# Optimization experiments

Measured on AMD Instinct MI355X. Metric: run time of the kernel, lower is better.

The kernel has to match this reference:

```python
import jax, jax.numpy as jnp
import numpy as np

ATT_DIM = 512
HEADS = 8
HEAD_DIM = ATT_DIM // HEADS
D_IN = 512
LEFT_MASK = 256
RIGHT_MASK = 0
LARGE = 1e30


def pos_encoding(S, d):
    # Transformer-XL sinusoid table over relative positions S-1 .. -(S-1), length 2S-1.
    inv_freq = (1.0 / (10000.0 ** (np.arange(0, d, 2.0) / d))).astype(np.float32)
    pos = jnp.arange(S - 1, -S, -1, dtype=jnp.float32)          # [2S-1]
    ang = pos[:, None] * jnp.asarray(inv_freq)[None, :]          # [2S-1, d/2]
    # concat([sin, cos], -1) on a trailing singleton -> interleaved sin/cos per frequency
    return jnp.stack([jnp.sin(ang), jnp.cos(ang)], axis=-1).reshape(2 * S - 1, d)


def rel_shift(x):
    # x: [B, N, S, 2S-1] -> [B, N, S, S] with out[i, j] = x[i, S-1 - i + j]
    B, N, S, L = x.shape
    x = jnp.pad(x, ((0, 0), (0, 0), (0, 0), (1, 0)))             # [B,N,S,L+1]
    x = x.reshape(B, N, L + 1, S)[:, :, 1:, :]                   # [B,N,L,S]
    x = x.reshape(B, N, S, L)
    return x[:, :, :, :S]


def setup_inputs() -> dict:
    key = jax.random.key(0)
    ks = jax.random.split(key, 9)
    B, S, D = 2, 2048, D_IN
    scale = 0.02
    return {
        "x": jax.random.normal(ks[0], (B, S, D), dtype=jnp.float32),
        "Wq": jax.random.normal(ks[1], (D, ATT_DIM), dtype=jnp.float32) * scale,
        "b_con": jax.random.normal(ks[2], (ATT_DIM,), dtype=jnp.float32) * scale,
        "b_rel": jax.random.normal(ks[3], (ATT_DIM,), dtype=jnp.float32) * scale,
        "Wk": jax.random.normal(ks[4], (D, ATT_DIM), dtype=jnp.float32) * scale,
        "Wkr": jax.random.normal(ks[5], (D_IN, ATT_DIM), dtype=jnp.float32) * scale,
        "Wv": jax.random.normal(ks[6], (D, ATT_DIM), dtype=jnp.float32) * scale,
        "bv": jax.random.normal(ks[7], (ATT_DIM,), dtype=jnp.float32) * scale,
        "x_len": jax.random.randint(ks[8], (B,), 1, S + 1).astype(jnp.int32),
    }


def reference(x, Wq, b_con, b_rel, Wk, Wkr, Wv, bv, x_len):
    B, S, D = x.shape
    N, Dh = HEADS, HEAD_DIM

    # content/relative query share the kernel (TiedDense) with separate biases
    q_lin = jnp.einsum('bsd,de->bse', x, Wq)
    q_con = (q_lin + b_con).reshape(B, S, N, Dh)
    q_rel = (q_lin + b_rel).reshape(B, S, N, Dh)
    k_con = jnp.einsum('bsd,de->bse', x, Wk).reshape(B, S, N, Dh)

    content_energy = jnp.einsum('bind,bjnd->bnij', q_con, k_con)  # [B,N,S,S]

    pos_emb = pos_encoding(S, D_IN)                               # [2S-1, D]
    k_rel = (pos_emb @ Wkr).reshape(2 * S - 1, N, Dh)
    relative_energy = jnp.einsum('bind,jnd->bnij', q_rel, k_rel)  # [B,N,S,2S-1]
    relative_energy = rel_shift(relative_energy)                  # [B,N,S,S]

    energy = (content_energy + relative_energy) / jnp.sqrt(jnp.float32(Dh))

    # sequence mask over keys (broadcast [B,1,1,S]) * banded mask (band_part)
    j = jnp.arange(S)
    seq_mask = (j[None, :] < x_len[:, None]).astype(jnp.float32)[:, None, None, :]
    i = jnp.arange(S)[:, None]
    band = ((i - j[None, :] <= LEFT_MASK) & (j[None, :] - i <= RIGHT_MASK)).astype(jnp.float32)
    mask = seq_mask * band[None, None, :, :]

    masked_energy = energy - (1.0 - mask) * LARGE
    attention = jax.nn.softmax(masked_energy, axis=-1)

    v = (jnp.einsum('bsd,de->bse', x, Wv) + bv).reshape(B, S, N, Dh)
    context = jnp.einsum('bnij,bjnd->bind', attention, v).reshape(B, S, N * Dh)
    return context
```

## Files before the change

### kernel.cpp

```cpp
#include <hip/hip_runtime.h>
#include <math.h>

#define S_ 2048
#define NH 8
#define DH 64
#define CSL 320
#define LP 72

typedef __attribute__((ext_vector_type(8))) short short8;
typedef __attribute__((ext_vector_type(4))) float f32x4;
typedef unsigned short ushort_t;

__device__ __forceinline__ short bf16r(float x) {
    union { float f; unsigned u; } v; v.f = x;
    unsigned r = v.u + 0x7fffu + ((v.u >> 16) & 1u);
    return (short)(r >> 16);
}
__device__ __forceinline__ float b2f(ushort_t h) {
    union { float f; unsigned u; } v; v.u = ((unsigned)h) << 16; return v.f;
}

__global__ __launch_bounds__(256) void prep_kernel(
    const float* __restrict__ x,
    const float* __restrict__ Wq, const float* __restrict__ Wk,
    const float* __restrict__ Wv, const float* __restrict__ Wkr,
    ushort_t* __restrict__ WTq, ushort_t* __restrict__ WTk,
    ushort_t* __restrict__ WTv, ushort_t* __restrict__ WTkr,
    ushort_t* __restrict__ pos, ushort_t* __restrict__ xb16)
{
    const int widx = blockIdx.z;
    const int t = threadIdx.x;
    if (widx == 4) {
        const int base = blockIdx.y * 8 + blockIdx.x;
        const float C = -0.051905126482615036f;
        const int f = t;
#pragma unroll
        for (int rep = 0; rep < 6; ++rep) {
            const int r = base + rep * 64;
            unsigned pk = 0;
            if (r <= 256) {
                float ang = (float)r * exp2f(C * (float)f);
                unsigned s = (unsigned)(ushort_t)bf16r(sinf(ang));
                unsigned c = (unsigned)(ushort_t)bf16r(cosf(ang));
                pk = s | (c << 16);
            }
            ((unsigned*)pos)[(size_t)r * 256 + f] = pk;
        }
        return;
    }
    if (widx == 5) {
        const int sub = blockIdx.y * 8 + blockIdx.x;
        const size_t base = (size_t)sub * 32768;
#pragma unroll
        for (int it = 0; it < 8; ++it) {
            const size_t idx = base + (size_t)it * 4096 + (size_t)t * 16;
            const float* src = &x[idx];
            ushort_t t16[16];
#pragma unroll
            for (int u = 0; u < 16; ++u) t16[u] = (ushort_t)bf16r(src[u]);
            *(short8*)&xb16[idx]     = *(short8*)&t16[0];
            *(short8*)&xb16[idx + 8] = *(short8*)&t16[8];
        }
        return;
    }
    const float* W = (widx == 0) ? Wq : (widx == 1) ? Wk : (widx == 2) ? Wv : Wkr;
    ushort_t* WT   = (widx == 0) ? WTq : (widx == 1) ? WTk : (widx == 2) ? WTv : WTkr;
    const int k0 = blockIdx.x * 64, n0 = blockIdx.y * 64;
    __shared__ __align__(16) ushort_t T[64][72];
    const int srow = t >> 2, sc0 = (t & 3) * 16;
    const float* src = &W[(size_t)(k0 + srow) * 512 + n0 + sc0];
#pragma unroll
    for (int u = 0; u < 16; ++u) T[sc0 + u][srow] = (ushort_t)bf16r(src[u]);
    __syncthreads();
    ushort_t* dst = &WT[(size_t)(n0 + srow) * 512 + k0 + sc0];
    *(short8*)dst       = *(const short8*)&T[srow][sc0];
    *(short8*)(dst + 8) = *(const short8*)&T[srow][sc0 + 8];
}

__global__ __launch_bounds__(256) void qkv_gemm(
    const ushort_t* __restrict__ xb16,
    const ushort_t* __restrict__ WTq, const ushort_t* __restrict__ WTk,
    const ushort_t* __restrict__ WTv,
    const ushort_t* __restrict__ pos, const ushort_t* __restrict__ WTkr,
    const float* __restrict__ b_con, const float* __restrict__ b_rel,
    const float* __restrict__ bv,
    ushort_t* __restrict__ qcon, ushort_t* __restrict__ qrel,
    ushort_t* __restrict__ kout, ushort_t* __restrict__ vT,
    ushort_t* __restrict__ krel)
{
    const int widx = blockIdx.y >> 3;
    const int tid = threadIdx.x, lane = tid & 63, w = tid >> 6;
    const int quad = lane >> 4, l16 = lane & 15;

    __shared__ __align__(16) ushort_t A_lds[128][40];
    __shared__ __align__(16) ushort_t B_lds[64][40];

    f32x4 acc[2][4];
#pragma unroll
    for (int mt = 0; mt < 2; ++mt)
#pragma unroll
        for (int nt = 0; nt < 4; ++nt) acc[mt][nt] = (f32x4){0.f, 0.f, 0.f, 0.f};

    const int arow = tid >> 1, ak0 = (tid & 1) * 16;
    const int brow = tid >> 2, bk0 = (tid & 3) * 8;

    if (widx < 2) {
        const int m0 = blockIdx.x * 128;
        const int n0 = (blockIdx.y & 7) * 64;
        const ushort_t* WT = (widx == 0) ? WTq : WTk;
        const ushort_t* xrow = &xb16[(size_t)(m0 + arow) * 512 + ak0];
        const ushort_t* wrow = &WT[(size_t)(n0 + brow) * 512 + bk0];

        short8 pa0 = *(const short8*)xrow;
        short8 pa1 = *(const short8*)(xrow + 8);
        short8 pb  = *(const short8*)wrow;

#pragma unroll 1
        for (int k0 = 0; k0 < 512; k0 += 32) {
            __syncthreads();
            *(short8*)&A_lds[arow][ak0]     = pa0;
            *(short8*)&A_lds[arow][ak0 + 8] = pa1;
            *(short8*)&B_lds[brow][bk0]     = pb;
            if (k0 < 480) {
                pa0 = *(const short8*)(xrow + k0 + 32);
                pa1 = *(const short8*)(xrow + k0 + 40);
                pb  = *(const short8*)(wrow + k0 + 32);
            }
            __syncthreads();
            short8 a0 = *(const short8*)&A_lds[w * 32 + l16][quad * 8];
            short8 a1 = *(const short8*)&A_lds[w * 32 + 16 + l16][quad * 8];
#pragma unroll
            for (int nt = 0; nt < 4; ++nt) {
                short8 bb = *(const short8*)&B_lds[nt * 16 + l16][quad * 8];
                acc[0][nt] = __builtin_amdgcn_mfma_f32_16x16x32_bf16(a0, bb, acc[0][nt], 0, 0, 0);
                acc[1][nt] = __builtin_amdgcn_mfma_f32_16x16x32_bf16(a1, bb, acc[1][nt], 0, 0, 0);
            }
        }

#pragma unroll
        for (int nt = 0; nt < 4; ++nt) {
            const int col = n0 + nt * 16 + l16;
            float bc = 0.f, br = 0.f;
            if (widx == 0) { bc = b_con[col]; br = b_rel[col]; }
#pragma unroll
            for (int mt = 0; mt < 2; ++mt) {
#pragma unroll
                for (int reg = 0; reg < 4; ++reg) {
                    const size_t m = (size_t)(m0 + w * 32 + mt * 16 + quad * 4 + reg);
                    const float val = acc[mt][nt][reg];
                    if (widx == 0) {
                        qcon[m * 512 + col] = (ushort_t)bf16r((val + bc) * 0.125f);
                        qrel[m * 512 + col] = (ushort_t)bf16r((val + br) * 0.125f);
                    } else {
                        kout[m * 512 + col] = (ushort_t)bf16r(val);
                    }
                }
            }
        }
    } else if (widx == 2) {
        const int vb = (blockIdx.y & 7) * 32 + blockIdx.x;
        const int m0d = (vb & 3) * 128;
        const int n0j = (vb >> 2) * 64;
        const ushort_t* wrow = &WTv[(size_t)(m0d + arow) * 512 + ak0];
        const ushort_t* xrow = &xb16[(size_t)(n0j + brow) * 512 + bk0];

        short8 pa0 = *(const short8*)wrow;
        short8 pa1 = *(const short8*)(wrow + 8);
        short8 pb  = *(const short8*)xrow;

#pragma unroll 1
        for (int k0 = 0; k0 < 512; k0 += 32) {
            __syncthreads();
            *(short8*)&A_lds[arow][ak0]     = pa0;
            *(short8*)&A_lds[arow][ak0 + 8] = pa1;
            *(short8*)&B_lds[brow][bk0]     = pb;
            if (k0 < 480) {
                pa0 = *(const short8*)(wrow + k0 + 32);
                pa1 = *(const short8*)(wrow + k0 + 40);
                pb  = *(const short8*)(xrow + k0 + 32);
            }
            __syncthreads();
            short8 a0 = *(const short8*)&A_lds[w * 32 + l16][quad * 8];
            short8 a1 = *(const short8*)&A_lds[w * 32 + 16 + l16][quad * 8];
#pragma unroll
            for (int nt = 0; nt < 4; ++nt) {
                short8 bb = *(const short8*)&B_lds[nt * 16 + l16][quad * 8];
                acc[0][nt] = __builtin_amdgcn_mfma_f32_16x16x32_bf16(a0, bb, acc[0][nt], 0, 0, 0);
                acc[1][nt] = __builtin_amdgcn_mfma_f32_16x16x32_bf16(a1, bb, acc[1][nt], 0, 0, 0);
            }
        }

        const int b = n0j >> 11;
#pragma unroll
        for (int mt = 0; mt < 2; ++mt) {
#pragma unroll
            for (int reg = 0; reg < 4; ++reg) {
                const int d = m0d + w * 32 + mt * 16 + quad * 4 + reg;
                const int n = d >> 6, dd = d & 63;
                const float bvv = bv[d];
#pragma unroll
                for (int nt = 0; nt < 4; ++nt) {
                    const int s = (n0j + nt * 16 + l16) & 2047;
                    vT[((size_t)((b * NH + n) * 64 + dd)) * 2048 + s] =
                        (ushort_t)bf16r(acc[mt][nt][reg] + bvv);
                }
            }
        }
    } else {
        if (blockIdx.x >= 24) return;
        const int m0 = (blockIdx.x >> 3) * 128;
        const int n0 = (blockIdx.x & 7) * 64;
        const ushort_t* prow = &pos[(size_t)(m0 + arow) * 512 + ak0];
        const ushort_t* wrow = &WTkr[(size_t)(n0 + brow) * 512 + bk0];

        short8 pa0 = *(const short8*)prow;
        short8 pa1 = *(const short8*)(prow + 8);
        short8 pb  = *(const short8*)wrow;

#pragma unroll 1
        for (int k0 = 0; k0 < 512; k0 += 32) {
            __syncthreads();
            *(short8*)&A_lds[arow][ak0]     = pa0;
            *(short8*)&A_lds[arow][ak0 + 8] = pa1;
            *(short8*)&B_lds[brow][bk0]     = pb;
            if (k0 < 480) {
                pa0 = *(const short8*)(prow + k0 + 32);
                pa1 = *(const short8*)(prow + k0 + 40);
                pb  = *(const short8*)(wrow + k0 + 32);
            }
            __syncthreads();
            short8 a0 = *(const short8*)&A_lds[w * 32 + l16][quad * 8];
            short8 a1 = *(const short8*)&A_lds[w * 32 + 16 + l16][quad * 8];
#pragma unroll
            for (int nt = 0; nt < 4; ++nt) {
                short8 bb = *(const short8*)&B_lds[nt * 16 + l16][quad * 8];
                acc[0][nt] = __builtin_amdgcn_mfma_f32_16x16x32_bf16(a0, bb, acc[0][nt], 0, 0, 0);
                acc[1][nt] = __builtin_amdgcn_mfma_f32_16x16x32_bf16(a1, bb, acc[1][nt], 0, 0, 0);
            }
        }

#pragma unroll
        for (int nt = 0; nt < 4; ++nt) {
            const int col = n0 + nt * 16 + l16;
#pragma unroll
            for (int mt = 0; mt < 2; ++mt)
#pragma unroll
                for (int reg = 0; reg < 4; ++reg) {
                    const size_t m = (size_t)(m0 + w * 32 + mt * 16 + quad * 4 + reg);
                    krel[m * 512 + col] = (ushort_t)bf16r(acc[mt][nt][reg]);
                }
        }
    }
}

__global__ __launch_bounds__(256) void rel_gemm(
    const ushort_t* __restrict__ qrel, const ushort_t* __restrict__ krel,
    const ushort_t* __restrict__ vT, ushort_t* __restrict__ R3,
    float* __restrict__ vmean)
{
    const int tile = blockIdx.x, n = blockIdx.y, b = blockIdx.z;
    const int tid = threadIdx.x, lane = tid & 63, w = tid >> 6;
    const int quad = lane >> 4, l16 = lane & 15;

    __shared__ __align__(16) ushort_t A_lds[128][LP];
    __shared__ __align__(16) ushort_t B_lds[64][LP];

    if (tile == 16) {
        const int row = tid >> 2, seg = tid & 3;
        const ushort_t* src = &vT[((size_t)((b * NH + n) * 64 + row)) * 2048 + seg * 512];
        float sum = 0.f;
        for (int it = 0; it < 64; ++it) {
            short8 h = *(const short8*)(src + it * 8);
#pragma unroll
            for (int u = 0; u < 8; ++u) sum += b2f((ushort_t)h[u]);
        }
        float* scratch = (float*)A_lds;
        scratch[row * 4 + seg] = sum;
        __syncthreads();
        if (tid < 64) {
            float s = scratch[tid * 4] + scratch[tid * 4 + 1]
                    + scratch[tid * 4 + 2] + scratch[tid * 4 + 3];
            vmean[(size_t)b * 512 + n * 64 + tid] = s * (1.0f / (float)S_);
        }
        return;
    }

    const int i0 = tile * 128;
    {
        const int srow = tid >> 1, sc0 = (tid & 1) * 32;
        const ushort_t* src = &qrel[((size_t)b * S_ + i0 + srow) * 512 + n * 64 + sc0];
#pragma unroll
        for (int u = 0; u < 4; ++u)
            *(short8*)&A_lds[srow][sc0 + u * 8] = *(const short8*)(src + u * 8);
    }

    const size_t rbase3 = (size_t)(b * NH + n) * S_ * CSL;
    const int srow2 = tid >> 2, sc2 = (tid & 3) * 16;

    short8 pb0, pb1;
    auto issueB = [&](int rc) {
        const ushort_t* src = &krel[(size_t)(rc * 64 + srow2) * 512 + n * 64 + sc2];
        pb0 = *(const short8*)src;
        pb1 = *(const short8*)(src + 8);
    };
    issueB(0);

#pragma unroll 1
    for (int rc = 0; rc < 5; ++rc) {
        __syncthreads();
        *(short8*)&B_lds[srow2][sc2]     = pb0;
        *(short8*)&B_lds[srow2][sc2 + 8] = pb1;
        if (rc < 4) issueB(rc + 1);
        __syncthreads();

        short8 a[2][2];
#pragma unroll
        for (int mt = 0; mt < 2; ++mt) {
            a[mt][0] = *(const short8*)&A_lds[w * 32 + mt * 16 + l16][quad * 8];
            a[mt][1] = *(const short8*)&A_lds[w * 32 + mt * 16 + l16][quad * 8 + 32];
        }
#pragma unroll
        for (int nt = 0; nt < 4; ++nt) {
            short8 b0 = *(const short8*)&B_lds[nt * 16 + l16][quad * 8];
            short8 b1 = *(const short8*)&B_lds[nt * 16 + l16][quad * 8 + 32];
            const int r = rc * 64 + nt * 16 + l16;
#pragma unroll
            for (int mt = 0; mt < 2; ++mt) {
                f32x4 s = (f32x4){0.f, 0.f, 0.f, 0.f};
                s = __builtin_amdgcn_mfma_f32_16x16x32_bf16(a[mt][0], b0, s, 0, 0, 0);
                s = __builtin_amdgcn_mfma_f32_16x16x32_bf16(a[mt][1], b1, s, 0, 0, 0);
                if (r <= 256) {
#pragma unroll
                    for (int reg = 0; reg < 4; ++reg) {
                        const int ig = i0 + w * 32 + mt * 16 + quad * 4 + reg;
                        const int cslot = (ig & 31) + 256 - r;
                        R3[rbase3 + (size_t)ig * CSL + cslot] = (ushort_t)bf16r(s[reg]);
                    }
                }
            }
        }
    }
}

__global__ __launch_bounds__(128) void attn_kernel(
    const ushort_t* __restrict__ qcon, const ushort_t* __restrict__ kbuf,
    const ushort_t* __restrict__ vT, const ushort_t* __restrict__ R3,
    const float* __restrict__ vmean, const int* __restrict__ xlen_p,
    float* __restrict__ out)
{
    const int bx = blockIdx.x;
    const int tile = ((bx & 7) << 3) | (bx >> 3);
    const int n = blockIdx.y, b = blockIdx.z;
    const int i0 = tile * 32;
    const int tid = threadIdx.x, lane = tid & 63, w = tid >> 6;
    const int quad = lane >> 4, l16 = lane & 15;
    const int xlen = xlen_p[b];

    __shared__ __align__(16) ushort_t q_lds[32][LP];
    __shared__ __align__(16) ushort_t k_lds[64][LP];
    __shared__ __align__(16) ushort_t vT_lds[64][LP];
    __shared__ __align__(16) ushort_t p_lds[32][LP];
    __shared__ __align__(16) ushort_t Rl_lds[32][LP];

    {
        const int qr = tid >> 2, qc = (tid & 3) * 16;
        const ushort_t* src = &qcon[((size_t)b * S_ + i0 + qr) * 512 + n * 64 + qc];
        *(short8*)&q_lds[qr][qc]     = *(const short8*)src;
        *(short8*)&q_lds[qr][qc + 8] = *(const short8*)(src + 8);
    }

    f32x4 Oa[4];
#pragma unroll
    for (int nt = 0; nt < 4; ++nt) Oa[nt] = (f32x4){0.f, 0.f, 0.f, 0.f};
    float lpart[4] = {};

    const size_t rbase3 = (size_t)(b * NH + n) * S_ * CSL;
    const size_t vTbase = (size_t)((b * NH + n) * 64) * 2048;
    const int srow = tid >> 1, sc0 = (tid & 1) * 32;
    const int rrow = tid >> 2, rcol = (tid & 3) * 16;
    const short8 z8 = {0, 0, 0, 0, 0, 0, 0, 0};

    short8 kr[4], vr[4], kn[4], vn[4];
    short8 rcur[2], rnxt[2];

    auto issue = [&](int c, short8* kd, short8* vd, short8* rd) {
        const int jc0 = i0 - 256 + c * 64;
        const int jg = jc0 + srow;
        const bool okk = (jg >= 0);
        const ushort_t* ks = &kbuf[((size_t)b * S_ + jg) * 512 + n * 64 + sc0];
        const ushort_t* vs = &vT[vTbase + (size_t)srow * 2048 + jc0 + sc0];
#pragma unroll
        for (int u = 0; u < 4; ++u) {
            kd[u] = okk ? *(const short8*)(ks + u * 8) : z8;
            const bool okv = (jc0 + sc0 + u * 8) >= 0;
            vd[u] = okv ? *(const short8*)(vs + u * 8) : z8;
        }
        const ushort_t* Rs = &R3[rbase3 + (size_t)(i0 + rrow) * CSL + c * 64 + rcol];
        rd[0] = *(const short8*)Rs;
        rd[1] = *(const short8*)(Rs + 8);
    };

    issue(0, kr, vr, rcur);

#pragma unroll 1
    for (int c = 0; c < 5; ++c) {
        const int jc0 = i0 - 256 + c * 64;
        __syncthreads();
#pragma unroll
        for (int u = 0; u < 4; ++u) {
            *(short8*)&k_lds[srow][sc0 + u * 8]  = kr[u];
            *(short8*)&vT_lds[srow][sc0 + u * 8] = vr[u];
        }
        *(short8*)&Rl_lds[rrow][rcol]     = rcur[0];
        *(short8*)&Rl_lds[rrow][rcol + 8] = rcur[1];
        if (c < 4) issue(c + 1, kn, vn, rnxt);
        __syncthreads();

        short8 aq0 = *(const short8*)&q_lds[w * 16 + l16][quad * 8];
        short8 aq1 = *(const short8*)&q_lds[w * 16 + l16][quad * 8 + 32];
        f32x4 Sacc[4];
#pragma unroll
        for (int jt = 0; jt < 4; ++jt) {
            short8 bk0 = *(const short8*)&k_lds[jt * 16 + l16][quad * 8];
            short8 bk1 = *(const short8*)&k_lds[jt * 16 + l16][quad * 8 + 32];
            f32x4 s = (f32x4){0.f, 0.f, 0.f, 0.f};
            s = __builtin_amdgcn_mfma_f32_16x16x32_bf16(aq0, bk0, s, 0, 0, 0);
            s = __builtin_amdgcn_mfma_f32_16x16x32_bf16(aq1, bk1, s, 0, 0, 0);
            Sacc[jt] = s;
        }

#pragma unroll
        for (int jt = 0; jt < 4; ++jt) {
#pragma unroll
            for (int reg = 0; reg < 4; ++reg) {
                const int row = w * 16 + quad * 4 + reg;
                const int i = i0 + row;
                const int j = jc0 + jt * 16 + l16;
                const int r = i - j;
                const bool valid = (j >= 0) && (j < xlen) && (r >= 0) && (r <= 256);
                float rvv = b2f(Rl_lds[row][jt * 16 + l16]);
                float e = valid ? __expf(Sacc[jt][reg] + rvv) : 0.f;
                lpart[reg] += e;
                p_lds[row][jt * 16 + l16] = (ushort_t)bf16r(e);
            }
        }
        __syncthreads();

        short8 ap0 = *(const short8*)&p_lds[w * 16 + l16][quad * 8];
        short8 ap1 = *(const short8*)&p_lds[w * 16 + l16][quad * 8 + 32];
#pragma unroll
        for (int nt = 0; nt < 4; ++nt) {
            short8 bv0 = *(const short8*)&vT_lds[nt * 16 + l16][quad * 8];
            short8 bv1 = *(const short8*)&vT_lds[nt * 16 + l16][quad * 8 + 32];
            Oa[nt] = __builtin_amdgcn_mfma_f32_16x16x32_bf16(ap0, bv0, Oa[nt], 0, 0, 0);
            Oa[nt] = __builtin_amdgcn_mfma_f32_16x16x32_bf16(ap1, bv1, Oa[nt], 0, 0, 0);
        }

#pragma unroll
        for (int u = 0; u < 4; ++u) { kr[u] = kn[u]; vr[u] = vn[u]; }
        rcur[0] = rnxt[0]; rcur[1] = rnxt[1];
    }

#pragma unroll
    for (int reg = 0; reg < 4; ++reg) {
#pragma unroll
        for (int off = 1; off < 16; off <<= 1)
            lpart[reg] += __shfl_xor(lpart[reg], off, 64);
    }

#pragma unroll
    for (int reg = 0; reg < 4; ++reg) {
        const int i = i0 + w * 16 + quad * 4 + reg;
        const bool dead = (i >= xlen + 256);
        const float linv = 1.0f / lpart[reg];
#pragma unroll
        for (int nt = 0; nt < 4; ++nt) {
            const int d = n * 64 + nt * 16 + l16;
            float val = dead ? vmean[(size_t)b * 512 + d] : Oa[nt][reg] * linv;
            out[((size_t)b * S_ + i) * 512 + d] = val;
        }
    }
}

extern "C" void kernel_launch(void* const* d_in, const int* in_sizes, int n_in,
                              void* d_out, int out_size, void* d_ws, size_t ws_size,
                              hipStream_t stream) {
    const float* x     = (const float*)d_in[0];
    const float* Wq    = (const float*)d_in[1];
    const float* b_con = (const float*)d_in[2];
    const float* b_rel = (const float*)d_in[3];
    const float* Wk    = (const float*)d_in[4];
    const float* Wkr   = (const float*)d_in[5];
    const float* Wv    = (const float*)d_in[6];
    const float* bv    = (const float*)d_in[7];
    const int*   xlen  = (const int*)d_in[8];
    float* out = (float*)d_out;

    float* ws = (float*)d_ws;
    float* vmean = ws;
    ushort_t* ub   = (ushort_t*)(vmean + 1024);
    ushort_t* R3   = ub;
    ushort_t* qcon = R3   + 10485760;
    ushort_t* kbuf = qcon + 2097152;
    ushort_t* vT   = kbuf + 2097152;
    ushort_t* qrel = vT   + 2097152;
    ushort_t* xb16 = qrel + 2097152;
    ushort_t* krel = xb16 + 2097152;
    ushort_t* pos  = krel + 196608;
    ushort_t* WTq  = pos  + 196608;
    ushort_t* WTk  = WTq + 262144;
    ushort_t* WTv  = WTk + 262144;
    ushort_t* WTkr = WTv + 262144;

    prep_kernel<<<dim3(8, 8, 6), 256, 0, stream>>>(x, Wq, Wk, Wv, Wkr,
                                                   WTq, WTk, WTv, WTkr, pos, xb16);
    qkv_gemm<<<dim3(32, 25), 256, 0, stream>>>(xb16, WTq, WTk, WTv, pos, WTkr,
                                               b_con, b_rel, bv,
                                               qcon, qrel, kbuf, vT, krel);
    rel_gemm<<<dim3(17, 8, 2), 256, 0, stream>>>(qrel, krel, vT, R3, vmean);
    attn_kernel<<<dim3(64, 8, 2), 128, 0, stream>>>(qcon, kbuf, vT, R3, vmean,
                                                    xlen, out);
}
```

Measured before the change: 136.3 us.

## Skip fully masked query tiles and key chunks using x_len

Uses per-batch x_len to skip work that the mask makes irrelevant. The Q/K GEMM and rel_gemm blocks return early for rows past xlen+256. In attn_kernel, tiles beyond that bound write the mean of V directly, because all their keys are masked and softmax becomes uniform over every key. Other tiles trim the number of key chunks to those below xlen. This depends on the reference mask semantics (uniform softmax when everything is masked) and ties runtime to the distribution of x_len.

Measured after the change: 131.1 us. 3.8% less time.

```diff
diff --git a/kernel.cpp b/kernel.cpp
--- a/kernel.cpp
+++ b/kernel.cpp
@@ -83,7 +83,7 @@
     const ushort_t* __restrict__ WTv,
     const ushort_t* __restrict__ pos, const ushort_t* __restrict__ WTkr,
     const float* __restrict__ b_con, const float* __restrict__ b_rel,
-    const float* __restrict__ bv,
+    const float* __restrict__ bv, const int* __restrict__ xlen_p,
     ushort_t* __restrict__ qcon, ushort_t* __restrict__ qrel,
     ushort_t* __restrict__ kout, ushort_t* __restrict__ vT,
     ushort_t* __restrict__ krel)
@@ -106,6 +106,12 @@
 
     if (widx < 2) {
         const int m0 = blockIdx.x * 128;
+        {
+            const int xl = xlen_p[m0 >> 11];
+            const int s0 = m0 & 2047;
+            if (widx == 0) { if (s0 >= xl + 256) return; }
+            else           { if (s0 >= xl + 63)  return; }
+        }
         const int n0 = (blockIdx.y & 7) * 64;
         const ushort_t* WT = (widx == 0) ? WTq : WTk;
         const ushort_t* xrow = &xb16[(size_t)(m0 + arow) * 512 + ak0];
@@ -255,8 +261,8 @@
 
 __global__ __launch_bounds__(256) void rel_gemm(
     const ushort_t* __restrict__ qrel, const ushort_t* __restrict__ krel,
-    const ushort_t* __restrict__ vT, ushort_t* __restrict__ R3,
-    float* __restrict__ vmean)
+    const ushort_t* __restrict__ vT, const int* __restrict__ xlen_p,
+    ushort_t* __restrict__ R3, float* __restrict__ vmean)
 {
     const int tile = blockIdx.x, n = blockIdx.y, b = blockIdx.z;
     const int tid = threadIdx.x, lane = tid & 63, w = tid >> 6;
@@ -286,6 +292,8 @@
     }
 
     const int i0 = tile * 128;
+    if (i0 >= xlen_p[b] + 256) return;
+
     {
         const int srow = tid >> 1, sc0 = (tid & 1) * 32;
         const ushort_t* src = &qrel[((size_t)b * S_ + i0 + srow) * 512 + n * 64 + sc0];
@@ -356,6 +364,18 @@
     const int quad = lane >> 4, l16 = lane & 15;
     const int xlen = xlen_p[b];
 
+    if (i0 >= xlen + 256) {
+        const int row = tid >> 2, c0 = (tid & 3) * 16;
+        const float* vm = &vmean[(size_t)b * 512 + n * 64 + c0];
+        float* dst = &out[((size_t)b * S_ + i0 + row) * 512 + n * 64 + c0];
+#pragma unroll
+        for (int u = 0; u < 16; u += 4)
+            *(float4*)&dst[u] = *(const float4*)&vm[u];
+        return;
+    }
+    int nchunk = (xlen - i0 + 256 + 63) >> 6;
+    if (nchunk > 5) nchunk = 5;
+
     __shared__ __align__(16) ushort_t q_lds[32][LP];
     __shared__ __align__(16) ushort_t k_lds[64][LP];
     __shared__ __align__(16) ushort_t vT_lds[64][LP];
@@ -403,7 +423,7 @@
     issue(0, kr, vr, rcur);
 
 #pragma unroll 1
-    for (int c = 0; c < 5; ++c) {
+    for (int c = 0; c < nchunk; ++c) {
         const int jc0 = i0 - 256 + c * 64;
         __syncthreads();
 #pragma unroll
@@ -413,7 +433,7 @@
         }
         *(short8*)&Rl_lds[rrow][rcol]     = rcur[0];
         *(short8*)&Rl_lds[rrow][rcol + 8] = rcur[1];
-        if (c < 4) issue(c + 1, kn, vn, rnxt);
+        if (c + 1 < nchunk) issue(c + 1, kn, vn, rnxt);
         __syncthreads();
 
         short8 aq0 = *(const short8*)&q_lds[w * 16 + l16][quad * 8];
@@ -515,9 +535,9 @@
     prep_kernel<<<dim3(8, 8, 6), 256, 0, stream>>>(x, Wq, Wk, Wv, Wkr,
                                                    WTq, WTk, WTv, WTkr, pos, xb16);
     qkv_gemm<<<dim3(32, 25), 256, 0, stream>>>(xb16, WTq, WTk, WTv, pos, WTkr,
-                                               b_con, b_rel, bv,
+                                               b_con, b_rel, bv, xlen,
                                                qcon, qrel, kbuf, vT, krel);
-    rel_gemm<<<dim3(17, 8, 2), 256, 0, stream>>>(qrel, krel, vT, R3, vmean);
+    rel_gemm<<<dim3(17, 8, 2), 256, 0, stream>>>(qrel, krel, vT, xlen, R3, vmean);
     attn_kernel<<<dim3(64, 8, 2), 128, 0, stream>>>(qcon, kbuf, vT, R3, vmean,
                                                     xlen, out);
 }
```
